# Performance work log

Hardware: AMD Instinct MI355X
Metric: run time of the kernel (lower is better)

The kernel has to match this reference:

```python
import jax, jax.numpy as jnp
import numpy as np

B, C, T, F = 8, 256, 256, 128
D, H, HEADS, K = 64, 128, 4, 8
I = D * K  # unfold channel dim = D*8


def _conv2d(x, w, b, stride=1, pad=0):
    y = jax.lax.conv_general_dilated(x, w, (stride, stride), [(pad, pad), (pad, pad)],
                                     dimension_numbers=('NCHW', 'OIHW', 'NCHW'))
    return y + b[None, :, None, None]


def _convT(x, w, b, strides):
    y = jax.lax.conv_transpose(x, w, strides, 'VALID', dimension_numbers=('NCHW', 'OIHW', 'NCHW'))
    return y + b[None, :, None, None]


def _sru_dir(x, Wx, bf, br, Whw):
    # x: (N, L, I). SRU: all matmuls precomputed, only elementwise recurrence in scan.
    u = jnp.einsum('nli,ih->nlh', x, Wx)  # (N, L, 3H)
    xt, fp, rp = jnp.split(u, 3, axis=-1)
    f = jax.nn.sigmoid(fp + bf)
    r = jax.nn.sigmoid(rp + br)
    xhw = jnp.einsum('nli,ih->nlh', x, Whw)  # highway projection (I != H)

    def step(c, inp):
        xt_t, f_t, r_t, xhw_t = inp
        c = f_t * c + (1.0 - f_t) * xt_t
        h = r_t * c + (1.0 - r_t) * xhw_t
        return c, h

    c0 = jnp.zeros((x.shape[0], bf.shape[-1]), x.dtype)
    seq = tuple(jnp.swapaxes(a, 0, 1) for a in (xt, f, r, xhw))  # (L, N, H)
    _, hs = jax.lax.scan(step, c0, seq)
    return jnp.swapaxes(hs, 0, 1)  # (N, L, H)


def _sru_bidir(x, Wx, bf, br, Whw):
    hf = _sru_dir(x, Wx[0], bf[0], br[0], Whw[0])
    hb = _sru_dir(x[:, ::-1], Wx[1], bf[1], br[1], Whw[1])[:, ::-1]
    return jnp.concatenate([hf, hb], axis=-1)  # (N, L, 2H)


def _unfold_last(x, k):
    # nn.Unfold(kernel=(1,k)) over last axis: (B,D,T,F) -> (B, D*k, T, F-k+1)
    L = x.shape[-1] - k + 1
    p = jnp.stack([x[..., i:i + L] for i in range(k)], axis=2)  # (B, D, k, T, L)
    b, d = x.shape[0], x.shape[1]
    return p.reshape(b, d * k, x.shape[2], L)


def _pathway(ag, Wx, bf, br, Whw, pw, pb, ctw, ctb):
    # unfold -> bidirectional SRU over last axis -> proj -> ConvTranspose2d(I->D, kernel (1,8))
    b, d, t, f = ag.shape
    L = f - K + 1
    u = _unfold_last(ag, K)                                  # (B, I, t, L)
    seq = u.transpose(0, 2, 3, 1).reshape(b * t, L, d * K)   # scan along unfolded axis
    h = _sru_bidir(seq, Wx, bf, br, Whw)                     # (b*t, L, 2H)
    z = h @ pw + pb                                          # (b*t, L, I)
    z = z.reshape(b, t, L, d * K).transpose(0, 3, 1, 2)      # (B, I, t, L)
    return _convT(z, ctw, ctb, (1, 1))                       # (B, D, t, f)


def _attention(x, qkv_w, qkv_b, ow, ob):
    b, d, t, f = x.shape
    n = t * f
    tok = x.reshape(b, d, n).transpose(0, 2, 1)  # (B, N, D)
    qkv = tok @ qkv_w + qkv_b
    q, k, v = jnp.split(qkv, 3, axis=-1)
    dh = d // HEADS
    sp = lambda a: a.reshape(b, n, HEADS, dh).transpose(0, 2, 1, 3)
    q, k, v = sp(q), sp(k), sp(v)
    s = jnp.einsum('bhnd,bhmd->bhnm', q, k) / jnp.sqrt(jnp.asarray(dh, x.dtype))
    a = jax.nn.softmax(s, axis=-1)
    o = jnp.einsum('bhnm,bhmd->bhnd', a, v).transpose(0, 2, 1, 3).reshape(b, n, d)
    o = o @ ow + ob
    return o.transpose(0, 2, 1).reshape(b, d, t, f)


def _forward(A, compress_w, compress_b, down_w0, down_b0, down_w1, down_b1,
             f_Wx, f_bf, f_br, f_Whw, f_proj_w, f_proj_b, f_ct_w, f_ct_b,
             t_Wx, t_bf, t_br, t_Whw, t_proj_w, t_proj_b, t_ct_w, t_ct_b,
             qkv_w, qkv_b, out_w, out_b, up_w0, up_b0, up_w1, up_b1, final_w, final_b):
    # Compressor: 1x1 conv C->D then 2 strided downsample units
    x0 = _conv2d(A, compress_w, compress_b)                              # (B,D,T,F)
    x1 = jax.nn.relu(_conv2d(x0, down_w0, down_b0, stride=2, pad=1))     # (B,D,T/2,F/2)
    x2 = jax.nn.relu(_conv2d(x1, down_w1, down_b1, stride=2, pad=1))     # (B,D,T/4,F/4)
    ag = x2
    # Dual path: frequency scan then time scan, with residuals as in _dual_path
    freq_out = _pathway(ag, f_Wx, f_bf, f_br, f_Whw, f_proj_w, f_proj_b, f_ct_w, f_ct_b) + ag
    agt = ag.transpose(0, 1, 3, 2)  # scan over time axis
    time_out = _pathway(agt, t_Wx, t_bf, t_br, t_Whw, t_proj_w, t_proj_b, t_ct_w, t_ct_b).transpose(0, 1, 3, 2) + freq_out
    # TF self-attention with residual
    dp = _attention(time_out, qkv_w, qkv_b, out_w, out_b) + time_out
    # U-Net style reconstruction with skips, project back to C
    y = _convT(dp, up_w0, up_b0, (2, 2)) + x1
    y = _convT(y, up_w1, up_b1, (2, 2)) + x0
    return _conv2d(y, final_w, final_b)                                  # (B,C,T,F)


def setup_inputs() -> dict:
    key = jax.random.key(0)
    ks = iter(jax.random.split(key, 64))

    def p(shape, scale=0.05):
        return jax.random.normal(next(ks), shape, dtype=jnp.float32) * scale

    inp = dict(
        A=jax.random.normal(next(ks), (B, C, T, F), dtype=jnp.float32),
        compress_w=p((D, C, 1, 1)), compress_b=p((D,)),
        down_w0=p((D, D, 3, 3)), down_b0=p((D,)),
        down_w1=p((D, D, 3, 3)), down_b1=p((D,)),
        f_Wx=p((2, I, 3 * H)), f_bf=p((2, H)), f_br=p((2, H)), f_Whw=p((2, I, H)),
        f_proj_w=p((2 * H, I)), f_proj_b=p((I,)), f_ct_w=p((D, I, 1, K)), f_ct_b=p((D,)),
        t_Wx=p((2, I, 3 * H)), t_bf=p((2, H)), t_br=p((2, H)), t_Whw=p((2, I, H)),
        t_proj_w=p((2 * H, I)), t_proj_b=p((I,)), t_ct_w=p((D, I, 1, K)), t_ct_b=p((D,)),
        qkv_w=p((D, 3 * D)), qkv_b=p((3 * D,)), out_w=p((D, D)), out_b=p((D,)),
        up_w0=p((D, D, 2, 2)), up_b0=p((D,)),
        up_w1=p((D, D, 2, 2)), up_b1=p((D,)),
        final_w=p((C, D, 1, 1)), final_b=p((C,)),
    )
    return inp


def reference(A, compress_w, compress_b, down_w0, down_b0, down_w1, down_b1,
              f_Wx, f_bf, f_br, f_Whw, f_proj_w, f_proj_b, f_ct_w, f_ct_b,
              t_Wx, t_bf, t_br, t_Whw, t_proj_w, t_proj_b, t_ct_w, t_ct_b,
              qkv_w, qkv_b, out_w, out_b, up_w0, up_b0, up_w1, up_b1, final_w, final_b):
    return _forward(A, compress_w, compress_b, down_w0, down_b0, down_w1, down_b1,
                    f_Wx, f_bf, f_br, f_Whw, f_proj_w, f_proj_b, f_ct_w, f_ct_b,
                    t_Wx, t_bf, t_br, t_Whw, t_proj_w, t_proj_b, t_ct_w, t_ct_b,
                    qkv_w, qkv_b, out_w, out_b, up_w0, up_b0, up_w1, up_b1, final_w, final_b)
```

## Files before the change

### kernel.cpp

```cpp
#include <hip/hip_runtime.h>

#define BB 8
#define CC 256
#define TT 256
#define FF 128
#define DD 64
#define HH 128
#define NHEADS 4
#define KK 8
#define II 512
#define T2 128
#define F2 64
#define T4 64
#define F4 32
#define P4 2048

#define LF 25
#define LT 57
#define MF (512*LF)
#define MT (256*LT)

typedef __attribute__((ext_vector_type(8))) short bf16x8;
typedef __attribute__((ext_vector_type(4))) float f32x4;

__device__ __forceinline__ ushort f2b(float x) {
    unsigned u = __float_as_uint(x);
    unsigned r = (u + 0x7FFFu + ((u >> 16) & 1u)) >> 16;
    return (ushort)r;
}
__device__ __forceinline__ float b2f(ushort x) {
    return __uint_as_float(((unsigned)x) << 16);
}
__device__ __forceinline__ unsigned cvtpk_bf16(float lo, float hi) {
    unsigned r;
    asm("v_cvt_pk_bf16_f32 %0, %1, %2" : "=v"(r) : "v"(lo), "v"(hi));
    return r;
}

__global__ __launch_bounds__(256) void mfma_gemm_k(
    const ushort* __restrict__ A16, const ushort* __restrict__ BT16,
    float* __restrict__ C, ushort* __restrict__ C16,
    const float* __restrict__ bias,
    int M, int N, int K, int out16)
{
    __shared__ ushort As[128][40];
    __shared__ ushort Bs[128][40];
    int m0 = blockIdx.y * 128, n0 = blockIdx.x * 128;
    int tid = threadIdx.x;
    int wave = tid >> 6, lane = tid & 63;
    int wm = (wave & 1) * 64, wn = (wave >> 1) * 64;
    int l15 = lane & 15, lhi = lane >> 4;
    f32x4 acc[4][4] = {};
    int rs = tid >> 2, qs = tid & 3;

    for (int k0 = 0; k0 < K; k0 += 32) {
        *(uint4*)&As[rs][qs * 8]      = *(const uint4*)(A16 + (long long)(m0 + rs) * K + k0 + qs * 8);
        *(uint4*)&As[rs + 64][qs * 8] = *(const uint4*)(A16 + (long long)(m0 + rs + 64) * K + k0 + qs * 8);
        *(uint4*)&Bs[rs][qs * 8]      = *(const uint4*)(BT16 + (long long)(n0 + rs) * K + k0 + qs * 8);
        *(uint4*)&Bs[rs + 64][qs * 8] = *(const uint4*)(BT16 + (long long)(n0 + rs + 64) * K + k0 + qs * 8);
        __syncthreads();
        bf16x8 af[4], bfr[4];
#pragma unroll
        for (int fr = 0; fr < 4; ++fr)
            af[fr] = *(const bf16x8*)&As[wm + fr * 16 + l15][lhi * 8];
#pragma unroll
        for (int fc = 0; fc < 4; ++fc)
            bfr[fc] = *(const bf16x8*)&Bs[wn + fc * 16 + l15][lhi * 8];
#pragma unroll
        for (int fr = 0; fr < 4; ++fr)
#pragma unroll
            for (int fc = 0; fc < 4; ++fc)
                acc[fr][fc] = __builtin_amdgcn_mfma_f32_16x16x32_bf16(af[fr], bfr[fc], acc[fr][fc], 0, 0, 0);
        __syncthreads();
    }
#pragma unroll
    for (int fr = 0; fr < 4; ++fr) {
#pragma unroll
        for (int fc = 0; fc < 4; ++fc) {
            int col = n0 + wn + fc * 16 + l15;
            float bv = bias ? bias[col] : 0.f;
#pragma unroll
            for (int r = 0; r < 4; ++r) {
                int row = m0 + wm + fr * 16 + lhi * 4 + r;
                float v = acc[fr][fc][r] + bv;
                long long ci = (long long)row * N + col;
                if (out16) C16[ci] = f2b(v);
                else       C[ci] = v;
            }
        }
    }
}

template<int BN>
__global__ __launch_bounds__(256) void mfma_nchw_k(
    const float* __restrict__ X, const ushort* __restrict__ WT,
    const float* __restrict__ bias, float* __restrict__ Y,
    int P, int N, int K)
{
    constexpr int FC = BN / 32;
    __shared__ ushort As[128][40];
    int p0 = blockIdx.x * 128;
    int n0 = blockIdx.y * BN;
    int b  = blockIdx.z;
    int tid = threadIdx.x, wave = tid >> 6, lane = tid & 63;
    int l15 = lane & 15, lhi = lane >> 4;
    int wm = (wave & 1) * 64, wn = (wave >> 1) * (BN / 2);
    f32x4 acc[4][FC] = {};
    const float* Xb = X + (long long)b * K * P;
    int kk_s = tid >> 3, pq_s = tid & 7;

    for (int k0 = 0; k0 < K; k0 += 32) {
        const float* xr = Xb + (long long)(k0 + kk_s) * P + p0;
#pragma unroll
        for (int j = 0; j < 4; ++j) {
            float4 v = *(const float4*)(xr + j * 32 + pq_s * 4);
            int pp = j * 32 + pq_s * 4;
            As[pp][kk_s]     = f2b(v.x);
            As[pp + 1][kk_s] = f2b(v.y);
            As[pp + 2][kk_s] = f2b(v.z);
            As[pp + 3][kk_s] = f2b(v.w);
        }
        __syncthreads();
        bf16x8 af[4], bfr[FC];
#pragma unroll
        for (int fr = 0; fr < 4; ++fr)
            af[fr] = *(const bf16x8*)&As[wm + fr * 16 + l15][lhi * 8];
#pragma unroll
        for (int fc = 0; fc < FC; ++fc)
            bfr[fc] = *(const bf16x8*)(WT + (long long)(n0 + wn + fc * 16 + l15) * K + k0 + lhi * 8);
#pragma unroll
        for (int fr = 0; fr < 4; ++fr)
#pragma unroll
            for (int fc = 0; fc < FC; ++fc)
                acc[fr][fc] = __builtin_amdgcn_mfma_f32_16x16x32_bf16(af[fr], bfr[fc], acc[fr][fc], 0, 0, 0);
        __syncthreads();
    }
#pragma unroll
    for (int fc = 0; fc < FC; ++fc) {
        int n = n0 + wn + fc * 16 + l15;
        float bv = bias[n];
        float* yr = Y + ((long long)(b * N + n)) * P + p0 + wm + lhi * 4;
#pragma unroll
        for (int fr = 0; fr < 4; ++fr) {
            float4 o;
            o.x = acc[fr][fc][0] + bv;
            o.y = acc[fr][fc][1] + bv;
            o.z = acc[fr][fc][2] + bv;
            o.w = acc[fr][fc][3] + bv;
            *(float4*)(yr + fr * 16) = o;
        }
    }
}

__global__ __launch_bounds__(256) void down_mfma_k(
    const float* __restrict__ in, const ushort* __restrict__ WT9,
    const float* __restrict__ bias, float* __restrict__ out,
    int Hi, int Wi)
{
    __shared__ ushort Is[289][64];
    int Ho = Hi >> 1, Wo = Wi >> 1;
    int ntx = Wo >> 3, nty = Ho >> 3;
    int tx = blockIdx.x % ntx; int rest = blockIdx.x / ntx;
    int ty = rest % nty; int b = rest / nty;
    int oy0 = ty * 8, ox0 = tx * 8;
    int iy0 = oy0 * 2 - 1, ix0 = ox0 * 2 - 1;
    int tid = threadIdx.x, wave = tid >> 6, lane = tid & 63;
    int l15 = lane & 15, lhi = lane >> 4;
    int wm = (wave & 1) * 32, wn = (wave >> 1) * 32;

    const float* ib = in + (long long)b * 64 * Hi * Wi;
    for (int i = tid; i < 289 * 64; i += 256) {
        int c = i / 289; int sp = i - c * 289;
        int r = sp / 17; int s = sp - r * 17;
        int iy = iy0 + r, ix = ix0 + s;
        float v = 0.f;
        if (iy >= 0 && iy < Hi && ix >= 0 && ix < Wi)
            v = ib[(long long)c * Hi * Wi + (long long)iy * Wi + ix];
        Is[sp][c ^ ((sp & 7) << 3)] = f2b(v);
    }
    __syncthreads();

    f32x4 acc[2][2] = {};
#pragma unroll
    for (int tap = 0; tap < 9; ++tap) {
        int kh = tap / 3, kw = tap - kh * 3;
#pragma unroll
        for (int half = 0; half < 2; ++half) {
            int c0 = half * 32 + lhi * 8;
            bf16x8 af[2], bw[2];
#pragma unroll
            for (int fr = 0; fr < 2; ++fr) {
                int p = wm + fr * 16 + l15;
                int sp = (2 * (p >> 3) + kh) * 17 + 2 * (p & 7) + kw;
                af[fr] = *(const bf16x8*)&Is[sp][c0 ^ ((sp & 7) << 3)];
            }
#pragma unroll
            for (int fc = 0; fc < 2; ++fc) {
                int d = wn + fc * 16 + l15;
                bw[fc] = *(const bf16x8*)(WT9 + (tap * 64 + d) * 64 + c0);
            }
#pragma unroll
            for (int fr = 0; fr < 2; ++fr)
#pragma unroll
                for (int fc = 0; fc < 2; ++fc)
                    acc[fr][fc] = __builtin_amdgcn_mfma_f32_16x16x32_bf16(af[fr], bw[fc], acc[fr][fc], 0, 0, 0);
        }
    }
#pragma unroll
    for (int fc = 0; fc < 2; ++fc) {
        int d = wn + fc * 16 + l15;
        float bv = bias[d];
        long long obase = ((long long)(b * 64 + d)) * Ho * Wo;
#pragma unroll
        for (int fr = 0; fr < 2; ++fr) {
#pragma unroll
            for (int r = 0; r < 4; ++r) {
                int p = wm + fr * 16 + lhi * 4 + r;
                int py = p >> 3, px = p & 7;
                out[obase + (long long)(oy0 + py) * Wo + ox0 + px] =
                    fmaxf(acc[fr][fc][r] + bv, 0.f);
            }
        }
    }
}

__global__ void pack_dw9_k(const float* __restrict__ w, ushort* __restrict__ O)
{
    int gid = blockIdx.x * blockDim.x + threadIdx.x;
    if (gid >= 9 * 64 * 64) return;
    int c = gid & 63; int rest = gid >> 6;
    int d = rest & 63; int tap = rest >> 6;
    O[gid] = f2b(w[(d * 64 + c) * 9 + tap]);
}

__global__ __launch_bounds__(256) void up_mfma_k(
    const float* __restrict__ in, const ushort* __restrict__ WT,
    const float* __restrict__ bias, const float* __restrict__ resid,
    float* __restrict__ out, int P, int wsh )
{
    __shared__ ushort As[128][72];
    int p0 = blockIdx.x * 128;
    int n0 = blockIdx.y * 128;
    int b  = blockIdx.z;
    int tid = threadIdx.x, wave = tid >> 6, lane = tid & 63;
    int l15 = lane & 15, lhi = lane >> 4;
    int wm = (wave & 1) * 64, wn = (wave >> 1) * 64;
    int Wi = 1 << wsh;
    int Ho = ((P >> wsh) << 1), Wo = Wi << 1;

    int kk_s = tid >> 3, pq_s = tid & 7;
#pragma unroll
    for (int h = 0; h < 2; ++h) {
        int k = h * 32 + kk_s;
        const float* xr = in + ((long long)(b * 64 + k)) * P + p0 + pq_s * 16;
#pragma unroll
        for (int j = 0; j < 4; ++j) {
            float4 v = *(const float4*)(xr + j * 4);
            int pp = pq_s * 16 + j * 4;
            As[pp][k]     = f2b(v.x);
            As[pp + 1][k] = f2b(v.y);
            As[pp + 2][k] = f2b(v.z);
            As[pp + 3][k] = f2b(v.w);
        }
    }
    __syncthreads();

    f32x4 acc[4][4] = {};
#pragma unroll
    for (int c = 0; c < 2; ++c) {
        bf16x8 af[4], bfr[4];
#pragma unroll
        for (int fr = 0; fr < 4; ++fr)
            af[fr] = *(const bf16x8*)&As[wm + fr * 16 + l15][c * 32 + lhi * 8];
#pragma unroll
        for (int fc = 0; fc < 4; ++fc)
            bfr[fc] = *(const bf16x8*)(WT + (long long)(n0 + wn + fc * 16 + l15) * 64 + c * 32 + lhi * 8);
#pragma unroll
        for (int fr = 0; fr < 4; ++fr)
#pragma unroll
            for (int fc = 0; fc < 4; ++fc)
                acc[fr][fc] = __builtin_amdgcn_mfma_f32_16x16x32_bf16(af[fr], bfr[fc], acc[fr][fc], 0, 0, 0);
    }

#pragma unroll
    for (int fc = 0; fc < 4; ++fc) {
        int n = n0 + wn + fc * 16 + l15;
        int parity = n >> 6, d = n & 63;
        int py = parity >> 1, px = parity & 1;
        float bv = bias[d];
        const long long obase = ((long long)(b * 64 + d)) * Ho * Wo;
#pragma unroll
        for (int fr = 0; fr < 4; ++fr) {
#pragma unroll
            for (int r = 0; r < 4; ++r) {
                int p = p0 + wm + fr * 16 + lhi * 4 + r;
                int iy = p >> wsh, ix = p & (Wi - 1);
                long long oi = obase + (long long)(2 * iy + py) * Wo + 2 * ix + px;
                out[oi] = acc[fr][fc][r] + bv + resid[oi];
            }
        }
    }
}

__global__ __launch_bounds__(256) void mfma_qkv_k(
    const float* __restrict__ X, const ushort* __restrict__ WT,
    const float* __restrict__ bias, ushort* __restrict__ C16)
{
    __shared__ ushort As[128][72];
    int p0 = blockIdx.x * 128;
    int b  = blockIdx.z;
    int tid = threadIdx.x, wave = tid >> 6, lane = tid & 63;
    int l15 = lane & 15, lhi = lane >> 4;
    int wm = (wave & 1) * 64, wn = (wave >> 1) * 96;

    int kk_s = tid >> 3, pq_s = tid & 7;
#pragma unroll
    for (int h = 0; h < 2; ++h) {
        int k = h * 32 + kk_s;
        const float* xr = X + ((long long)(b * 64 + k)) * P4 + p0 + pq_s * 16;
#pragma unroll
        for (int j = 0; j < 4; ++j) {
            float4 v = *(const float4*)(xr + j * 4);
            int pp = pq_s * 16 + j * 4;
            As[pp][k]     = f2b(v.x);
            As[pp + 1][k] = f2b(v.y);
            As[pp + 2][k] = f2b(v.z);
            As[pp + 3][k] = f2b(v.w);
        }
    }
    __syncthreads();

    f32x4 acc[4][6] = {};
#pragma unroll
    for (int c = 0; c < 2; ++c) {
        bf16x8 af[4], bfr[6];
#pragma unroll
        for (int fr = 0; fr < 4; ++fr)
            af[fr] = *(const bf16x8*)&As[wm + fr * 16 + l15][c * 32 + lhi * 8];
#pragma unroll
        for (int fc = 0; fc < 6; ++fc)
            bfr[fc] = *(const bf16x8*)(WT + (long long)(wn + fc * 16 + l15) * 64 + c * 32 + lhi * 8);
#pragma unroll
        for (int fr = 0; fr < 4; ++fr)
#pragma unroll
            for (int fc = 0; fc < 6; ++fc)
                acc[fr][fc] = __builtin_amdgcn_mfma_f32_16x16x32_bf16(af[fr], bfr[fc], acc[fr][fc], 0, 0, 0);
    }
#pragma unroll
    for (int fc = 0; fc < 6; ++fc) {
        int n = wn + fc * 16 + l15;
        float bv = bias[n];
#pragma unroll
        for (int fr = 0; fr < 4; ++fr)
#pragma unroll
            for (int r = 0; r < 4; ++r) {
                int p = p0 + wm + fr * 16 + lhi * 4 + r;
                C16[((long long)(b * P4 + p)) * 192 + n] = f2b(acc[fr][fc][r] + bv);
            }
    }
}

__global__ __launch_bounds__(256) void mfma_attnout_k(
    const float* __restrict__ A, const ushort* __restrict__ owT,
    const float* __restrict__ ob, const float* __restrict__ resid,
    float* __restrict__ dp)
{
    __shared__ ushort As[128][72];
    int p0 = blockIdx.x * 128;
    int b  = blockIdx.z;
    int tid = threadIdx.x, wave = tid >> 6, lane = tid & 63;
    int l15 = lane & 15, lhi = lane >> 4;
    int wm = (wave & 1) * 64, wn = (wave >> 1) * 32;

    int rs = tid >> 2, qs = tid & 3;
#pragma unroll
    for (int h = 0; h < 2; ++h) {
        int row = h * 64 + rs;
        const float* ar = A + ((long long)(b * P4 + p0 + row)) * 64 + qs * 16;
#pragma unroll
        for (int j = 0; j < 4; ++j) {
            float4 v = *(const float4*)(ar + j * 4);
            int c = qs * 16 + j * 4;
            *(unsigned*)&As[row][c]     = cvtpk_bf16(v.x, v.y);
            *(unsigned*)&As[row][c + 2] = cvtpk_bf16(v.z, v.w);
        }
    }
    __syncthreads();

    f32x4 acc[4][2] = {};
#pragma unroll
    for (int c = 0; c < 2; ++c) {
        bf16x8 af[4], bfr[2];
#pragma unroll
        for (int fr = 0; fr < 4; ++fr)
            af[fr] = *(const bf16x8*)&As[wm + fr * 16 + l15][c * 32 + lhi * 8];
#pragma unroll
        for (int fc = 0; fc < 2; ++fc)
            bfr[fc] = *(const bf16x8*)(owT + (long long)(wn + fc * 16 + l15) * 64 + c * 32 + lhi * 8);
#pragma unroll
        for (int fr = 0; fr < 4; ++fr)
#pragma unroll
            for (int fc = 0; fc < 2; ++fc)
                acc[fr][fc] = __builtin_amdgcn_mfma_f32_16x16x32_bf16(af[fr], bfr[fc], acc[fr][fc], 0, 0, 0);
    }
#pragma unroll
    for (int fc = 0; fc < 2; ++fc) {
        int n = wn + fc * 16 + l15;
        float bv = ob[n];
        long long base = ((long long)(b * 64 + n)) * P4;
#pragma unroll
        for (int fr = 0; fr < 4; ++fr) {
            int p = p0 + wm + fr * 16 + lhi * 4;
            float4 rv = *(const float4*)(resid + base + p);
            float4 o;
            o.x = acc[fr][fc][0] + bv + rv.x;
            o.y = acc[fr][fc][1] + bv + rv.y;
            o.z = acc[fr][fc][2] + bv + rv.z;
            o.w = acc[fr][fc][3] + bv + rv.w;
            *(float4*)(dp + base + p) = o;
        }
    }
}

__global__ void pack_w16_k(const float* __restrict__ W, ushort* __restrict__ O, int n)
{
    int gid = blockIdx.x * blockDim.x + threadIdx.x;
    if (gid < n) O[gid] = f2b(W[gid]);
}
__global__ void pack_transposeT_k(const float* __restrict__ W, ushort* __restrict__ O,
                                  int K, int N)
{
    int gid = blockIdx.x * blockDim.x + threadIdx.x;
    if (gid >= K * N) return;
    int k = gid % K, n = gid / K;
    O[gid] = f2b(W[(long long)k * N + n]);
}
__global__ void pack_upw_k(const float* __restrict__ w, ushort* __restrict__ O)
{
    int gid = blockIdx.x * blockDim.x + threadIdx.x;
    if (gid >= 16384) return;
    int c = gid & 63; int n = gid >> 6;
    int parity = n >> 6, d = n & 63;
    int py = parity >> 1, px = parity & 1;
    O[gid] = f2b(w[((d * 64 + c) * 2 + (1 - py)) * 2 + (1 - px)]);
}

__global__ __launch_bounds__(256) void attn_mfma_k(const ushort* __restrict__ qkv,
                                                   float* __restrict__ out)
{
    __shared__ ushort Qs[128][40];
    __shared__ ushort Ks[64][40];
    __shared__ ushort VsT[16][72];
    __shared__ ushort Ps[128][72];
    int qt = blockIdx.x, h = blockIdx.y, b = blockIdx.z;
    int tid = threadIdx.x, wave = tid >> 6, lane = tid & 63;
    int l15 = lane & 15, lhi = lane >> 4;
    int q0 = wave * 32;

    for (int i = tid; i < 1024; i += 256) {
        int row = i >> 3, c = i & 7;
        *(unsigned*)&Qs[row][16 + c * 2] = 0u;
    }
    for (int i = tid; i < 512; i += 256) {
        int row = i >> 3, c = i & 7;
        *(unsigned*)&Ks[row][16 + c * 2] = 0u;
    }
    {
        const ushort* qp = qkv + ((long long)(b * P4 + qt * 128)) * 192 + h * 16;
        for (int i = tid; i < 2048; i += 256) {
            int row = i >> 4, d = i & 15;
            Qs[row][d] = f2b(b2f(qp[row * 192 + d]) * 0.25f);
        }
    }
    __syncthreads();

    float mmax[2] = {-1e30f, -1e30f};
    float lsum[2] = {0.f, 0.f};
    f32x4 oacc[2] = {};

    for (int k0 = 0; k0 < P4; k0 += 64) {
        const ushort* kp = qkv + ((long long)(b * P4 + k0)) * 192 + 64 + h * 16;
        for (int i = tid; i < 1024; i += 256) {
            int key = i >> 4, d = i & 15;
            Ks[key][d]  = kp[key * 192 + d];
            VsT[d][key] = kp[key * 192 + 64 + d];
        }
        __syncthreads();

        bf16x8 bq[2];
        bq[0] = *(const bf16x8*)&Qs[q0 + l15][lhi * 8];
        bq[1] = *(const bf16x8*)&Qs[q0 + 16 + l15][lhi * 8];
        f32x4 s[4][2];
#pragma unroll
        for (int fr = 0; fr < 4; ++fr) {
            bf16x8 ak = *(const bf16x8*)&Ks[fr * 16 + l15][lhi * 8];
            f32x4 z = {};
            s[fr][0] = __builtin_amdgcn_mfma_f32_16x16x32_bf16(ak, bq[0], z, 0, 0, 0);
            s[fr][1] = __builtin_amdgcn_mfma_f32_16x16x32_bf16(ak, bq[1], z, 0, 0, 0);
        }
#pragma unroll
        for (int fc = 0; fc < 2; ++fc) {
            float m = s[0][fc][0];
#pragma unroll
            for (int fr = 0; fr < 4; ++fr)
#pragma unroll
                for (int r = 0; r < 4; ++r) m = fmaxf(m, s[fr][fc][r]);
            m = fmaxf(m, __shfl_xor(m, 16));
            m = fmaxf(m, __shfl_xor(m, 32));
            float nm = fmaxf(mmax[fc], m);
            float corr = __expf(mmax[fc] - nm);
            mmax[fc] = nm;
            float ps = 0.f;
#pragma unroll
            for (int fr = 0; fr < 4; ++fr)
#pragma unroll
                for (int r = 0; r < 4; ++r) {
                    float p = __expf(s[fr][fc][r] - nm);
                    s[fr][fc][r] = p;
                    ps += p;
                }
            lsum[fc] = lsum[fc] * corr + ps;
#pragma unroll
            for (int r = 0; r < 4; ++r) oacc[fc][r] *= corr;
        }
#pragma unroll
        for (int fc = 0; fc < 2; ++fc)
#pragma unroll
            for (int fr = 0; fr < 4; ++fr) {
                uint2 pk;
                pk.x = cvtpk_bf16(s[fr][fc][0], s[fr][fc][1]);
                pk.y = cvtpk_bf16(s[fr][fc][2], s[fr][fc][3]);
                *(uint2*)&Ps[q0 + fc * 16 + l15][fr * 16 + lhi * 4] = pk;
            }
#pragma unroll
        for (int ks = 0; ks < 2; ++ks) {
            bf16x8 av = *(const bf16x8*)&VsT[l15][ks * 32 + lhi * 8];
#pragma unroll
            for (int fc = 0; fc < 2; ++fc) {
                bf16x8 bp = *(const bf16x8*)&Ps[q0 + fc * 16 + l15][ks * 32 + lhi * 8];
                oacc[fc] = __builtin_amdgcn_mfma_f32_16x16x32_bf16(av, bp, oacc[fc], 0, 0, 0);
            }
        }
        __syncthreads();
    }
#pragma unroll
    for (int fc = 0; fc < 2; ++fc) {
        float L = lsum[fc];
        L += __shfl_xor(L, 16);
        L += __shfl_xor(L, 32);
        float inv = 1.f / L;
        int q = qt * 128 + q0 + fc * 16 + l15;
        float* op = out + ((long long)(b * P4 + q)) * 64 + h * 16 + lhi * 4;
#pragma unroll
        for (int r = 0; r < 4; ++r) op[r] = oacc[fc][r] * inv;
    }
}

__global__ void convt_reduce_k(const float* __restrict__ Y, const float* __restrict__ bias,
                               const float* __restrict__ resid, float* __restrict__ out,
                               int NS, int L, int FO, int swap)
{
    int gid = blockIdx.x * blockDim.x + threadIdx.x;
    int total = BB * 64 * NS * FO;
    if (gid >= total) return;
    int d = gid & 63; int rest = gid >> 6;
    int p = rest % FO; rest /= FO;
    int s = rest % NS; int b = rest / NS;
    float v = bias[d];
    long long ybase = ((long long)(b * NS + s)) * L;
#pragma unroll
    for (int tap = 0; tap < 8; ++tap) {
        int l = p + tap - 7;
        if (l >= 0 && l < L) v += Y[(ybase + l) * 512 + tap * 64 + d];
    }
    long long oi = swap ? (((long long)(b * 64 + d) * FO + p) * NS + s)
                        : (((long long)(b * 64 + d) * NS + s) * FO + p);
    out[oi] = v + resid[oi];
}

__global__ void unfold_freq_k(const float* __restrict__ ag, ushort* __restrict__ u)
{
    long long gid = (long long)blockIdx.x * blockDim.x + threadIdx.x;
    if (gid >= (long long)MF * II) return;
    int ch = (int)(gid & 511); int row = (int)(gid >> 9);
    int b = row / (T4 * LF); int rem = row - b * (T4 * LF);
    int t = rem / LF; int l = rem - t * LF;
    int d = ch >> 3, i = ch & 7;
    u[gid] = f2b(ag[((long long)((b * DD + d) * T4 + t)) * F4 + l + i]);
}
__global__ void unfold_time_k(const float* __restrict__ ag, ushort* __restrict__ u)
{
    long long gid = (long long)blockIdx.x * blockDim.x + threadIdx.x;
    if (gid >= (long long)MT * II) return;
    int ch = (int)(gid & 511); int row = (int)(gid >> 9);
    int b = row / (F4 * LT); int rem = row - b * (F4 * LT);
    int tt = rem / LT; int l = rem - tt * LT;
    int d = ch >> 3, i = ch & 7;
    u[gid] = f2b(ag[((long long)((b * DD + d) * T4 + (l + i))) * F4 + tt]);
}

__global__ void pack_wcatT_k(const float* __restrict__ Wx, const float* __restrict__ Whw,
                             ushort* __restrict__ WT)
{
    int gid = blockIdx.x * blockDim.x + threadIdx.x;
    if (gid >= 1024 * 512) return;
    int k = gid & 511; int n = gid >> 9;
    int dir = n >> 9; int c = n & 511;
    float v = (c < 384) ? Wx[(dir * 512 + k) * 384 + c]
                        : Whw[(dir * 512 + k) * 128 + (c - 384)];
    WT[gid] = f2b(v);
}
__global__ void pack_pwT_k(const float* __restrict__ pw, ushort* __restrict__ WT)
{
    int gid = blockIdx.x * blockDim.x + threadIdx.x;
    if (gid >= 512 * 256) return;
    int k = gid & 255; int n = gid >> 8;
    WT[gid] = f2b(pw[k * 512 + n]);
}
__global__ void pack_wct2T_k(const float* __restrict__ ctw, ushort* __restrict__ WT)
{
    int gid = blockIdx.x * blockDim.x + threadIdx.x;
    if (gid >= 512 * 512) return;
    int k = gid & 511; int n = gid >> 9;
    int tap = n >> 6, d = n & 63;
    WT[gid] = f2b(ctw[((d * 512) + k) * 8 + tap]);
}

__global__ void sru_scan_k(const float* __restrict__ G, const float* __restrict__ bfw,
                           const float* __restrict__ brw, ushort* __restrict__ hout,
                           int Nn, int L)
{
    int gid = blockIdx.x * blockDim.x + threadIdx.x;
    if (gid >= Nn * 256) return;
    int h = gid & 127; int dir = (gid >> 7) & 1; int n = gid >> 8;
    const float bf = bfw[dir * 128 + h], br = brw[dir * 128 + h];
    int base = dir * 512 + h;
    float c = 0.f;
    for (int s = 0; s < L; ++s) {
        int l = dir ? (L - 1 - s) : s;
        const float* g = G + ((long long)(n * L + l)) * 1024 + base;
        float xt = g[0];
        float fv = 1.f / (1.f + __expf(-(g[128] + bf)));
        float rv = 1.f / (1.f + __expf(-(g[256] + br)));
        float xh = g[384];
        c = fv * c + (1.f - fv) * xt;
        float hv = rv * c + (1.f - rv) * xh;
        hout[((long long)(n * L + l)) * 256 + dir * 128 + h] = f2b(hv);
    }
}

extern "C" void kernel_launch(void* const* d_in, const int* in_sizes, int n_in,
                              void* d_out, int out_size, void* d_ws, size_t ws_size,
                              hipStream_t stream)
{
    const float* A_in  = (const float*)d_in[0];
    const float* cw    = (const float*)d_in[1];
    const float* cb    = (const float*)d_in[2];
    const float* dw0   = (const float*)d_in[3];
    const float* db0   = (const float*)d_in[4];
    const float* dw1   = (const float*)d_in[5];
    const float* db1   = (const float*)d_in[6];
    const float* f_Wx  = (const float*)d_in[7];
    const float* f_bf  = (const float*)d_in[8];
    const float* f_br  = (const float*)d_in[9];
    const float* f_Whw = (const float*)d_in[10];
    const float* f_pw  = (const float*)d_in[11];
    const float* f_pb  = (const float*)d_in[12];
    const float* f_ctw = (const float*)d_in[13];
    const float* f_ctb = (const float*)d_in[14];
    const float* t_Wx  = (const float*)d_in[15];
    const float* t_bf  = (const float*)d_in[16];
    const float* t_br  = (const float*)d_in[17];
    const float* t_Whw = (const float*)d_in[18];
    const float* t_pw  = (const float*)d_in[19];
    const float* t_pb  = (const float*)d_in[20];
    const float* t_ctw = (const float*)d_in[21];
    const float* t_ctb = (const float*)d_in[22];
    const float* qkv_w = (const float*)d_in[23];
    const float* qkv_b = (const float*)d_in[24];
    const float* ow    = (const float*)d_in[25];
    const float* ob    = (const float*)d_in[26];
    const float* upw0  = (const float*)d_in[27];
    const float* upb0  = (const float*)d_in[28];
    const float* upw1  = (const float*)d_in[29];
    const float* upb1  = (const float*)d_in[30];
    const float* fw    = (const float*)d_in[31];
    const float* fb    = (const float*)d_in[32];

    float* ws  = (float*)d_ws;
    float* out = (float*)d_out;

    float* ag    = ws + 0;
    float* x1    = ws + 1048576;
    float* Ureg  = ws + 5242880;
    float* G     = ws + 12713984;
    float* h16f  = ws + 27656192;
    float* z16f  = ws + 29523968;
    float* wcatf = ws + 33259520;
    float* wct2f = ws + 33521664;
    float* pwtf  = ws + 33652736;
    float* fout  = ws + 33718272;
    float* tout  = ws + 34766848;
    float* qkvbf = ws + 35815424;
    float* attnO = ws + 38961152;
    float* dp    = ws + 40009728;
    float* cw16f = ws + 41058304;
    float* fw16f = ws + 41066496;
    float* wup0f = ws + 41074688;
    float* wup1f = ws + 41082880;
    float* qkvwf = ws + 41091072;
    float* owtf  = ws + 41097216;
    float* wdw0f = ws + 41098240;
    float* wdw1f = ws + 41116672;
    ushort* u16    = (ushort*)Ureg;
    float*  Y      = Ureg;
    float*  y1     = Ureg;
    float*  y0     = G;
    ushort* h16    = (ushort*)h16f;
    ushort* z16    = (ushort*)z16f;
    ushort* WcatT  = (ushort*)wcatf;
    ushort* Wct2T  = (ushort*)wct2f;
    ushort* pwT    = (ushort*)pwtf;
    ushort* qkv16  = (ushort*)qkvbf;
    ushort* cw16   = (ushort*)cw16f;
    ushort* fw16   = (ushort*)fw16f;
    ushort* WupT0  = (ushort*)wup0f;
    ushort* WupT1  = (ushort*)wup1f;
    ushort* qkvwT  = (ushort*)qkvwf;
    ushort* owT    = (ushort*)owtf;
    ushort* WT9d0  = (ushort*)wdw0f;
    ushort* WT9d1  = (ushort*)wdw1f;
    float*  x0     = out;

    dim3 blk(256);

    pack_w16_k<<<dim3(64), blk, 0, stream>>>(cw, cw16, 16384);
    pack_w16_k<<<dim3(64), blk, 0, stream>>>(fw, fw16, 16384);
    pack_upw_k<<<dim3(64), blk, 0, stream>>>(upw0, WupT0);
    pack_upw_k<<<dim3(64), blk, 0, stream>>>(upw1, WupT1);
    pack_transposeT_k<<<dim3(48), blk, 0, stream>>>(qkv_w, qkvwT, 64, 192);
    pack_transposeT_k<<<dim3(16), blk, 0, stream>>>(ow, owT, 64, 64);
    pack_dw9_k<<<dim3(144), blk, 0, stream>>>(dw0, WT9d0);
    pack_dw9_k<<<dim3(144), blk, 0, stream>>>(dw1, WT9d1);

    mfma_nchw_k<64><<<dim3(256, 1, 8), blk, 0, stream>>>(A_in, cw16, cb, x0, 32768, 64, 256);

    down_mfma_k<<<dim3(1024), blk, 0, stream>>>(x0, WT9d0, db0, x1, TT, FF);
    down_mfma_k<<<dim3(256), blk, 0, stream>>>(x1, WT9d1, db1, ag, T2, F2);

    unfold_freq_k<<<dim3((MF * II) / 256), blk, 0, stream>>>(ag, u16);
    pack_wcatT_k<<<dim3(2048), blk, 0, stream>>>(f_Wx, f_Whw, WcatT);
    mfma_gemm_k<<<dim3(8, MF / 128), blk, 0, stream>>>(u16, WcatT, G, nullptr, nullptr,
        MF, 1024, 512, 0);
    sru_scan_k<<<dim3(131072 / 256), blk, 0, stream>>>(G, f_bf, f_br, h16, 512, LF);
    pack_pwT_k<<<dim3(512), blk, 0, stream>>>(f_pw, pwT);
    mfma_gemm_k<<<dim3(4, MF / 128), blk, 0, stream>>>(h16, pwT, nullptr, z16, f_pb,
        MF, 512, 256, 1);
    pack_wct2T_k<<<dim3(1024), blk, 0, stream>>>(f_ctw, Wct2T);
    mfma_gemm_k<<<dim3(4, MF / 128), blk, 0, stream>>>(z16, Wct2T, Y, nullptr, nullptr,
        MF, 512, 512, 0);
    convt_reduce_k<<<dim3(4096), blk, 0, stream>>>(Y, f_ctb, ag, fout, 64, LF, 32, 0);

    unfold_time_k<<<dim3((MT * II) / 256), blk, 0, stream>>>(ag, u16);
    pack_wcatT_k<<<dim3(2048), blk, 0, stream>>>(t_Wx, t_Whw, WcatT);
    mfma_gemm_k<<<dim3(8, MT / 128), blk, 0, stream>>>(u16, WcatT, G, nullptr, nullptr,
        MT, 1024, 512, 0);
    sru_scan_k<<<dim3(65536 / 256), blk, 0, stream>>>(G, t_bf, t_br, h16, 256, LT);
    pack_pwT_k<<<dim3(512), blk, 0, stream>>>(t_pw, pwT);
    mfma_gemm_k<<<dim3(4, MT / 128), blk, 0, stream>>>(h16, pwT, nullptr, z16, t_pb,
        MT, 512, 256, 1);
    pack_wct2T_k<<<dim3(1024), blk, 0, stream>>>(t_ctw, Wct2T);
    mfma_gemm_k<<<dim3(4, MT / 128), blk, 0, stream>>>(z16, Wct2T, Y, nullptr, nullptr,
        MT, 512, 512, 0);
    convt_reduce_k<<<dim3(4096), blk, 0, stream>>>(Y, t_ctb, fout, tout, 32, LT, 64, 1);

    mfma_qkv_k<<<dim3(16, 1, 8), blk, 0, stream>>>(tout, qkvwT, qkv_b, qkv16);
    attn_mfma_k<<<dim3(16, NHEADS, BB), blk, 0, stream>>>(qkv16, attnO);
    mfma_attnout_k<<<dim3(16, 1, 8), blk, 0, stream>>>(attnO, owT, ob, tout, dp);

    up_mfma_k<<<dim3(16, 2, 8), blk, 0, stream>>>(dp, WupT0, upb0, x1, y1, 2048, 5);
    up_mfma_k<<<dim3(64, 2, 8), blk, 0, stream>>>(y1, WupT1, upb1, x0, y0, 8192, 6);

    mfma_nchw_k<128><<<dim3(256, 2, 8), blk, 0, stream>>>(y0, fw16, fb, out, 32768, 256, 64);
}
```

Before: 709.7 us.

## Fold SRU projection into ConvTranspose weights and fuse gate sigmoids into GEMM

Precomputes a combined weight W3 = proj_w·ct_w (plus a folded bias) so each pathway runs one K=256 GEMM on h instead of two GEMMs (K=256 then K=512) with a bf16 intermediate z. The gate GEMM now applies the sigmoids in its epilogue and writes a compact layout: interleaved fp32 xt/xhw plus packed bf16 f/r, which cuts the bytes the scan has to read. B fragments in the new GEMMs are read straight from global memory instead of through shared memory. The cost is two extra rounds of bf16 rounding (on the fused weights and the gates), plus a small serial bias kernel.

Measured after the change: 902.4 us. 1.27x slower.

```diff
diff --git a/kernel.cpp b/kernel.cpp
--- a/kernel.cpp
+++ b/kernel.cpp
@@ -41,7 +41,7 @@
     const ushort* __restrict__ A16, const ushort* __restrict__ BT16,
     float* __restrict__ C, ushort* __restrict__ C16,
     const float* __restrict__ bias,
-    int M, int N, int K, int out16)
+    int M, int N, int K, int out16, int ctrans)
 {
     __shared__ ushort As[128][40];
     __shared__ ushort Bs[128][40];
@@ -83,12 +83,126 @@
             for (int r = 0; r < 4; ++r) {
                 int row = m0 + wm + fr * 16 + lhi * 4 + r;
                 float v = acc[fr][fc][r] + bv;
-                long long ci = (long long)row * N + col;
-                if (out16) C16[ci] = f2b(v);
-                else       C[ci] = v;
-            }
-        }
-    }
+                if (out16) {
+                    long long ci = ctrans ? ((long long)col * M + row) : ((long long)row * N + col);
+                    C16[ci] = f2b(v);
+                } else {
+                    C[(long long)row * N + col] = v;
+                }
+            }
+        }
+    }
+}
+
+__global__ __launch_bounds__(256) void gates_gemm_k(
+    const ushort* __restrict__ A16, const ushort* __restrict__ WT,
+    float* __restrict__ Gxh, ushort* __restrict__ Gfr,
+    const float* __restrict__ bfw, const float* __restrict__ brw, int M)
+{
+    __shared__ ushort As[128][40];
+    const int K = 512;
+    int m0 = blockIdx.y * 128, n0 = blockIdx.x * 128;
+    int tid = threadIdx.x, wave = tid >> 6, lane = tid & 63;
+    int wm = (wave & 1) * 64, wn = (wave >> 1) * 64;
+    int l15 = lane & 15, lhi = lane >> 4;
+    f32x4 acc[4][4] = {};
+    int rs = tid >> 2, qs = tid & 3;
+
+    for (int k0 = 0; k0 < K; k0 += 32) {
+        *(uint4*)&As[rs][qs * 8]      = *(const uint4*)(A16 + (long long)(m0 + rs) * K + k0 + qs * 8);
+        *(uint4*)&As[rs + 64][qs * 8] = *(const uint4*)(A16 + (long long)(m0 + rs + 64) * K + k0 + qs * 8);
+        __syncthreads();
+        bf16x8 af[4], bfr[4];
+#pragma unroll
+        for (int fr = 0; fr < 4; ++fr)
+            af[fr] = *(const bf16x8*)&As[wm + fr * 16 + l15][lhi * 8];
+#pragma unroll
+        for (int fc = 0; fc < 4; ++fc)
+            bfr[fc] = *(const bf16x8*)(WT + (long long)(n0 + wn + fc * 16 + l15) * K + k0 + lhi * 8);
+#pragma unroll
+        for (int fr = 0; fr < 4; ++fr)
+#pragma unroll
+            for (int fc = 0; fc < 4; ++fc)
+                acc[fr][fc] = __builtin_amdgcn_mfma_f32_16x16x32_bf16(af[fr], bfr[fc], acc[fr][fc], 0, 0, 0);
+        __syncthreads();
+    }
+#pragma unroll
+    for (int fc = 0; fc < 4; ++fc) {
+        int col = n0 + wn + fc * 16 + l15;
+        int dir = col >> 9, c = col & 511;
+        int cls = c >> 7, h = c & 127;
+        int dh = dir * 128 + h;
+#pragma unroll
+        for (int fr = 0; fr < 4; ++fr) {
+#pragma unroll
+            for (int r = 0; r < 4; ++r) {
+                int row = m0 + wm + fr * 16 + lhi * 4 + r;
+                long long idx = (long long)row * 256 + dh;
+                float v = acc[fr][fc][r];
+                if (cls == 0)      Gxh[idx * 2] = v;
+                else if (cls == 3) Gxh[idx * 2 + 1] = v;
+                else if (cls == 1) Gfr[idx * 2]     = f2b(1.f / (1.f + __expf(-(v + bfw[dh]))));
+                else               Gfr[idx * 2 + 1] = f2b(1.f / (1.f + __expf(-(v + brw[dh]))));
+            }
+        }
+    }
+}
+
+__global__ __launch_bounds__(256) void mfma_gemmW_k(
+    const ushort* __restrict__ A16, const ushort* __restrict__ WT,
+    float* __restrict__ C, const float* __restrict__ bias,
+    int M, int N, int K)
+{
+    __shared__ ushort As[128][40];
+    int m0 = blockIdx.y * 128, n0 = blockIdx.x * 128;
+    int tid = threadIdx.x, wave = tid >> 6, lane = tid & 63;
+    int wm = (wave & 1) * 64, wn = (wave >> 1) * 64;
+    int l15 = lane & 15, lhi = lane >> 4;
+    f32x4 acc[4][4] = {};
+    int rs = tid >> 2, qs = tid & 3;
+
+    for (int k0 = 0; k0 < K; k0 += 32) {
+        *(uint4*)&As[rs][qs * 8]      = *(const uint4*)(A16 + (long long)(m0 + rs) * K + k0 + qs * 8);
+        *(uint4*)&As[rs + 64][qs * 8] = *(const uint4*)(A16 + (long long)(m0 + rs + 64) * K + k0 + qs * 8);
+        __syncthreads();
+        bf16x8 af[4], bfr[4];
+#pragma unroll
+        for (int fr = 0; fr < 4; ++fr)
+            af[fr] = *(const bf16x8*)&As[wm + fr * 16 + l15][lhi * 8];
+#pragma unroll
+        for (int fc = 0; fc < 4; ++fc)
+            bfr[fc] = *(const bf16x8*)(WT + (long long)(n0 + wn + fc * 16 + l15) * K + k0 + lhi * 8);
+#pragma unroll
+        for (int fr = 0; fr < 4; ++fr)
+#pragma unroll
+            for (int fc = 0; fc < 4; ++fc)
+                acc[fr][fc] = __builtin_amdgcn_mfma_f32_16x16x32_bf16(af[fr], bfr[fc], acc[fr][fc], 0, 0, 0);
+        __syncthreads();
+    }
+#pragma unroll
+    for (int fc = 0; fc < 4; ++fc) {
+        int col = n0 + wn + fc * 16 + l15;
+        float bv = bias[col];
+#pragma unroll
+        for (int fr = 0; fr < 4; ++fr) {
+#pragma unroll
+            for (int r = 0; r < 4; ++r) {
+                int row = m0 + wm + fr * 16 + lhi * 4 + r;
+                C[(long long)row * N + col] = acc[fr][fc][r] + bv;
+            }
+        }
+    }
+}
+
+__global__ void bias3_k(const float* __restrict__ pb, const float* __restrict__ ctw,
+                        float* __restrict__ b3)
+{
+    int n = blockIdx.x * blockDim.x + threadIdx.x;
+    if (n >= 512) return;
+    int d = n & 63, tap = n >> 6;
+    float s = 0.f;
+    for (int i = 0; i < 512; ++i) s += pb[i] * ctw[(d * 512 + i) * 8 + tap];
+    b3[n] = s;
 }
 
 template<int BN>
@@ -610,13 +724,6 @@
                         : Whw[(dir * 512 + k) * 128 + (c - 384)];
     WT[gid] = f2b(v);
 }
-__global__ void pack_pwT_k(const float* __restrict__ pw, ushort* __restrict__ WT)
-{
-    int gid = blockIdx.x * blockDim.x + threadIdx.x;
-    if (gid >= 512 * 256) return;
-    int k = gid & 255; int n = gid >> 8;
-    WT[gid] = f2b(pw[k * 512 + n]);
-}
 __global__ void pack_wct2T_k(const float* __restrict__ ctw, ushort* __restrict__ WT)
 {
     int gid = blockIdx.x * blockDim.x + threadIdx.x;
@@ -626,26 +733,24 @@
     WT[gid] = f2b(ctw[((d * 512) + k) * 8 + tap]);
 }
 
-__global__ void sru_scan_k(const float* __restrict__ G, const float* __restrict__ bfw,
-                           const float* __restrict__ brw, ushort* __restrict__ hout,
-                           int Nn, int L)
+__global__ void sru_scan_k(const float* __restrict__ Gxh, const unsigned* __restrict__ Gfr,
+                           ushort* __restrict__ hout, int Nn, int L)
 {
     int gid = blockIdx.x * blockDim.x + threadIdx.x;
     if (gid >= Nn * 256) return;
     int h = gid & 127; int dir = (gid >> 7) & 1; int n = gid >> 8;
-    const float bf = bfw[dir * 128 + h], br = brw[dir * 128 + h];
-    int base = dir * 512 + h;
+    int dh = dir * 128 + h;
     float c = 0.f;
     for (int s = 0; s < L; ++s) {
         int l = dir ? (L - 1 - s) : s;
-        const float* g = G + ((long long)(n * L + l)) * 1024 + base;
-        float xt = g[0];
-        float fv = 1.f / (1.f + __expf(-(g[128] + bf)));
-        float rv = 1.f / (1.f + __expf(-(g[256] + br)));
-        float xh = g[384];
-        c = fv * c + (1.f - fv) * xt;
-        float hv = rv * c + (1.f - rv) * xh;
-        hout[((long long)(n * L + l)) * 256 + dir * 128 + h] = f2b(hv);
+        long long off = (long long)(n * L + l) * 256 + dh;
+        float xt = Gxh[off * 2], xh = Gxh[off * 2 + 1];
+        unsigned fr = Gfr[off];
+        float f = b2f((ushort)(fr & 0xffff));
+        float r = b2f((ushort)(fr >> 16));
+        c = f * c + (1.f - f) * xt;
+        float hv = r * c + (1.f - r) * xh;
+        hout[off] = f2b(hv);
     }
 }
 
@@ -693,12 +798,14 @@
     float* ag    = ws + 0;
     float* x1    = ws + 1048576;
     float* Ureg  = ws + 5242880;
-    float* G     = ws + 12713984;
+    float* Gxh   = ws + 12713984;
+    float* Gfrf  = ws + 20185088;
     float* h16f  = ws + 27656192;
-    float* z16f  = ws + 29523968;
+    float* pw16f = ws + 29523968;
+    float* w3tf  = ws + 29589504;
+    float* b3f   = ws + 29655040;
     float* wcatf = ws + 33259520;
     float* wct2f = ws + 33521664;
-    float* pwtf  = ws + 33652736;
     float* fout  = ws + 33718272;
     float* tout  = ws + 34766848;
     float* qkvbf = ws + 35815424;
@@ -715,12 +822,14 @@
     ushort* u16    = (ushort*)Ureg;
     float*  Y      = Ureg;
     float*  y1     = Ureg;
-    float*  y0     = G;
+    float*  y0     = Gxh;
+    unsigned* Gfr32 = (unsigned*)Gfrf;
+    ushort* Gfr16  = (ushort*)Gfrf;
     ushort* h16    = (ushort*)h16f;
-    ushort* z16    = (ushort*)z16f;
+    ushort* pw16   = (ushort*)pw16f;
+    ushort* W3T    = (ushort*)w3tf;
     ushort* WcatT  = (ushort*)wcatf;
     ushort* Wct2T  = (ushort*)wct2f;
-    ushort* pwT    = (ushort*)pwtf;
     ushort* qkv16  = (ushort*)qkvbf;
     ushort* cw16   = (ushort*)cw16f;
     ushort* fw16   = (ushort*)fw16f;
@@ -750,28 +859,26 @@
 
     unfold_freq_k<<<dim3((MF * II) / 256), blk, 0, stream>>>(ag, u16);
     pack_wcatT_k<<<dim3(2048), blk, 0, stream>>>(f_Wx, f_Whw, WcatT);
-    mfma_gemm_k<<<dim3(8, MF / 128), blk, 0, stream>>>(u16, WcatT, G, nullptr, nullptr,
-        MF, 1024, 512, 0);
-    sru_scan_k<<<dim3(131072 / 256), blk, 0, stream>>>(G, f_bf, f_br, h16, 512, LF);
-    pack_pwT_k<<<dim3(512), blk, 0, stream>>>(f_pw, pwT);
-    mfma_gemm_k<<<dim3(4, MF / 128), blk, 0, stream>>>(h16, pwT, nullptr, z16, f_pb,
-        MF, 512, 256, 1);
+    gates_gemm_k<<<dim3(8, MF / 128), blk, 0, stream>>>(u16, WcatT, Gxh, Gfr16, f_bf, f_br, MF);
+    sru_scan_k<<<dim3(131072 / 256), blk, 0, stream>>>(Gxh, Gfr32, h16, 512, LF);
+    pack_w16_k<<<dim3(512), blk, 0, stream>>>(f_pw, pw16, 131072);
     pack_wct2T_k<<<dim3(1024), blk, 0, stream>>>(f_ctw, Wct2T);
-    mfma_gemm_k<<<dim3(4, MF / 128), blk, 0, stream>>>(z16, Wct2T, Y, nullptr, nullptr,
-        MF, 512, 512, 0);
+    mfma_gemm_k<<<dim3(4, 2), blk, 0, stream>>>(pw16, Wct2T, nullptr, W3T, nullptr,
+        256, 512, 512, 1, 1);
+    bias3_k<<<dim3(2), blk, 0, stream>>>(f_pb, f_ctw, b3f);
+    mfma_gemmW_k<<<dim3(4, MF / 128), blk, 0, stream>>>(h16, W3T, Y, b3f, MF, 512, 256);
     convt_reduce_k<<<dim3(4096), blk, 0, stream>>>(Y, f_ctb, ag, fout, 64, LF, 32, 0);
 
     unfold_time_k<<<dim3((MT * II) / 256), blk, 0, stream>>>(ag, u16);
     pack_wcatT_k<<<dim3(2048), blk, 0, stream>>>(t_Wx, t_Whw, WcatT);
-    mfma_gemm_k<<<dim3(8, MT / 128), blk, 0, stream>>>(u16, WcatT, G, nullptr, nullptr,
-        MT, 1024, 512, 0);
-    sru_scan_k<<<dim3(65536 / 256), blk, 0, stream>>>(G, t_bf, t_br, h16, 256, LT);
-    pack_pwT_k<<<dim3(512), blk, 0, stream>>>(t_pw, pwT);
-    mfma_gemm_k<<<dim3(4, MT / 128), blk, 0, stream>>>(h16, pwT, nullptr, z16, t_pb,
-        MT, 512, 256, 1);
+    gates_gemm_k<<<dim3(8, MT / 128), blk, 0, stream>>>(u16, WcatT, Gxh, Gfr16, t_bf, t_br, MT);
+    sru_scan_k<<<dim3(65536 / 256), blk, 0, stream>>>(Gxh, Gfr32, h16, 256, LT);
+    pack_w16_k<<<dim3(512), blk, 0, stream>>>(t_pw, pw16, 131072);
     pack_wct2T_k<<<dim3(1024), blk, 0, stream>>>(t_ctw, Wct2T);
-    mfma_gemm_k<<<dim3(4, MT / 128), blk, 0, stream>>>(z16, Wct2T, Y, nullptr, nullptr,
-        MT, 512, 512, 0);
+    mfma_gemm_k<<<dim3(4, 2), blk, 0, stream>>>(pw16, Wct2T, nullptr, W3T, nullptr,
+        256, 512, 512, 1, 1);
+    bias3_k<<<dim3(2), blk, 0, stream>>>(t_pb, t_ctw, b3f);
+    mfma_gemmW_k<<<dim3(4, MT / 128), blk, 0, stream>>>(h16, W3T, Y, b3f, MT, 512, 256);
     convt_reduce_k<<<dim3(4096), blk, 0, stream>>>(Y, t_ctb, fout, tout, 32, LT, 64, 1);
 
     mfma_qkv_k<<<dim3(16, 1, 8), blk, 0, stream>>>(tout, qkvwT, qkv_b, qkv16);
```
